# Kernel tuning notes

Measured on AMD Instinct MI355X. Metric: run time of the kernel, lower is better.

The kernel has to match this reference:

```python
import jax, jax.numpy as jnp
import numpy as np
from jax import lax

BN_EPS = 1e-5


def setup_inputs() -> dict:
    key = jax.random.key(0)
    ks = jax.random.split(key, 3)
    B, N, D = 96, 20, 2048
    return {
        "x": jax.random.normal(ks[0], (B, N, D), dtype=jnp.float32),
        "conv_w": jax.random.normal(ks[1], (D, 2 * D), dtype=jnp.float32) * 0.02,
        "conv_b": jax.random.normal(ks[2], (D,), dtype=jnp.float32) * 0.02,
        "bn_gamma": jnp.ones((D,), dtype=jnp.float32),
        "bn_beta": jnp.zeros((D,), dtype=jnp.float32),
        "bn_mean": jnp.zeros((D,), dtype=jnp.float32),
        "bn_var": jnp.ones((D,), dtype=jnp.float32),
        "n_neighbor": 10,
    }


def reference(x, conv_w, conv_b, bn_gamma, bn_beta, bn_mean, bn_var, n_neighbor):
    # x: [B, N, D] -> xt: [B, D, N] (channels-first point cloud of view features)
    xt = jnp.transpose(x, (0, 2, 1))
    B, D, N = xt.shape
    k = int(n_neighbor)

    # pairwise squared distances: [B, N, N]
    sq = jnp.sum(xt * xt, axis=1, keepdims=True)            # [B, 1, N]
    inner = jnp.einsum("bdn,bdm->bnm", xt, xt)              # [B, N, N]
    adj = sq + (-2.0) * inner + jnp.transpose(sq, (0, 2, 1))

    # k nearest neighbors (smallest distance) -> idx [B, N, k]
    _, nn_idx = lax.top_k(-adj, k)

    # gather neighbor features without the O(N^2) expand: [B, D, N, k]
    neighbors = jax.vmap(lambda xb, idx: xb[:, idx])(xt, nn_idx)

    center = xt[:, :, :, None]                              # [B, D, N, 1]
    edge = jnp.concatenate(
        [jnp.broadcast_to(center, (B, D, N, k)), neighbors - center], axis=1
    )                                                       # [B, 2D, N, k]

    # 1x1 conv (GEMM over channel dim) + BatchNorm (inference) + ReLU
    y = jnp.einsum("oc,bcnk->bonk", conv_w, edge) + conv_b[None, :, None, None]
    inv = bn_gamma / jnp.sqrt(bn_var + BN_EPS)
    y = y * inv[None, :, None, None] + (bn_beta - bn_mean * inv)[None, :, None, None]
    y = jax.nn.relu(y)

    # max over neighbors, then max over points -> [B, D, 1, 1]
    y = jnp.max(y, axis=-1, keepdims=True)
    y = jnp.max(y, axis=2, keepdims=True)
    return y
```

## Files before the change

kernel.cpp:

```cpp
#include <hip/hip_runtime.h>
#include <hip/hip_bf16.h>
#include <math.h>

#define BN_EPS 1e-5f
#define B_  96
#define N_  20
#define D_  2048
#define K_  10
#define M_  (B_*N_)
#define R_  (2*D_)

typedef __attribute__((ext_vector_type(8))) short bf16x8;
typedef __attribute__((ext_vector_type(4))) float f32x4;
typedef __attribute__((ext_vector_type(8))) unsigned short ushort8;

static __device__ __forceinline__ unsigned short f2bf(float f) {
  unsigned int u = __builtin_bit_cast(unsigned int, f);
  u = u + 0x7fffu + ((u >> 16) & 1u);
  return (unsigned short)(u >> 16);
}

#define GLOAD_LDS16(g, l) \
  __builtin_amdgcn_global_load_lds((const __attribute__((address_space(1))) void*)(g), \
                                   (__attribute__((address_space(3))) void*)(l), 16, 0, 0)

__global__ __launch_bounds__(512) void knn_cast_kernel(const float* __restrict__ x,
                                                       int* __restrict__ nn_idx,
                                                       unsigned short* __restrict__ Xb)
{
  int b = blockIdx.x, t = threadIdx.x, w = t >> 6, lane = t & 63;
  __shared__ float innr[N_*N_];
  __shared__ float adjl[N_*N_];
  const float* xb = x + (size_t)b * N_ * D_;
  for (int p = w; p < (N_*(N_+1))/2; p += 8) {
    int n = 0;
    while ((n+1)*N_ - ((n+1)*n)/2 <= p) ++n;
    int m = n + (p - (n*N_ - (n*(n-1))/2));
    const float4* xn = (const float4*)(xb + n * D_);
    const float4* xm = (const float4*)(xb + m * D_);
    float s = 0.f;
    #pragma unroll
    for (int c = lane; c < D_/4; c += 64) {
      float4 a = xn[c], v = xm[c];
      s = fmaf(a.x, v.x, fmaf(a.y, v.y, fmaf(a.z, v.z, fmaf(a.w, v.w, s))));
    }
    #pragma unroll
    for (int off = 32; off > 0; off >>= 1)
      s += __shfl_xor(s, off, 64);
    if (lane == 0) { innr[n*N_+m] = s; innr[m*N_+n] = s; }
  }
  __syncthreads();
  for (int p = t; p < N_*N_; p += 512) {
    int n = p / N_, m = p % N_;
    adjl[p] = innr[n*N_+n] + innr[m*N_+m] - 2.f * innr[p];
  }
  __syncthreads();
  if (t < N_) {
    int n = t;
    unsigned mask = 0;
    for (int it = 0; it < K_; ++it) {
      float bv = INFINITY; int bi = 0;
      for (int m = 0; m < N_; ++m) {
        if (!((mask >> m) & 1u)) {
          float v = adjl[n*N_+m];
          if (v < bv) { bv = v; bi = m; }
        }
      }
      mask |= 1u << bi;
      nn_idx[(b*N_ + n)*K_ + it] = bi;
    }
  }
  unsigned short* xo = Xb + (size_t)b * N_ * D_;
  for (int i = t; i < N_*D_/8; i += 512) {
    const float4* src = (const float4*)xb + (size_t)i * 2;
    float4 a = src[0], c = src[1];
    ushort8 o = { f2bf(a.x), f2bf(a.y), f2bf(a.z), f2bf(a.w),
                  f2bf(c.x), f2bf(c.y), f2bf(c.z), f2bf(c.w) };
    *((ushort8*)xo + i) = o;
  }
}

__global__ __launch_bounds__(256) void cast_w_kernel(const float* __restrict__ cw,
                                                     unsigned short* __restrict__ Wn)
{
  int i = blockIdx.x * 256 + threadIdx.x;
  int r = i >> 8;
  int k = (i & 255) * 8;
  const float* src = cw + (size_t)(r >> 1) * R_ + ((r & 1) << 11) + k;
  float4 a = *(const float4*)src, c = *(const float4*)(src + 4);
  ushort8 o = { f2bf(a.x), f2bf(a.y), f2bf(a.z), f2bf(a.w),
                f2bf(c.x), f2bf(c.y), f2bf(c.z), f2bf(c.w) };
  *((ushort8*)Wn + i) = o;
}

__global__ __launch_bounds__(256, 4) void fused_gemm(
    const unsigned short* __restrict__ Xb, const unsigned short* __restrict__ Wn,
    const int* __restrict__ nn_idx, const float* __restrict__ conv_b,
    const float* __restrict__ gamma, const float* __restrict__ beta,
    const float* __restrict__ mean, const float* __restrict__ var,
    float* __restrict__ out)
{
  __shared__ __align__(16) char smem[44160];
  unsigned short* As = (unsigned short*)smem;
  unsigned short* Bs = (unsigned short*)(smem + 10240);
  float* Cl  = (float*)smem;
  int*   idxl = (int*)(smem + 40960);

  int flat = blockIdx.y * 24 + blockIdx.x;
  int nf = (flat & 7) * 96 + (flat >> 3);
  int bx = nf % 24, by = nf / 24;

  int t = threadIdx.x, lane = t & 63, w = t >> 6;
  int m0 = bx * 80, b0 = bx * 4;
  int r0 = by * 128, o0 = by * 64;
  int rowsel = lane & 15, ksel = lane >> 4;

  for (int i = t; i < 4*N_*K_; i += 256) idxl[i] = nn_idx[b0*N_*K_ + i];

  f32x4 acc[5][2] = {};

  for (int k0 = 0; k0 < D_; k0 += 64) {
    #pragma unroll
    for (int i = 0; i < 3; ++i) {
      int fl = i*256 + t;
      if (fl < 640) {
        int row = fl >> 3, kc = fl & 7;
        GLOAD_LDS16(Xb + (size_t)(m0 + row) * D_ + k0 + ((kc ^ (row & 7)) << 3),
                    As + fl*8);
      }
    }
    #pragma unroll
    for (int i = 0; i < 4; ++i) {
      int fl = i*256 + t;
      int row = fl >> 3, kc = fl & 7;
      GLOAD_LDS16(Wn + (size_t)(r0 + row) * D_ + k0 + ((kc ^ (row & 7)) << 3),
                  Bs + fl*8);
    }
    __syncthreads();
    #pragma unroll
    for (int ks = 0; ks < 2; ++ks) {
      int swz = ((ks*4 + ksel) ^ (rowsel & 7)) << 3;
      bf16x8 a[5], bfr[2];
      #pragma unroll
      for (int mi = 0; mi < 5; ++mi)
        a[mi] = *(const bf16x8*)(As + (mi*16 + rowsel)*64 + swz);
      #pragma unroll
      for (int ri = 0; ri < 2; ++ri)
        bfr[ri] = *(const bf16x8*)(Bs + (w*32 + ri*16 + rowsel)*64 + swz);
      #pragma unroll
      for (int mi = 0; mi < 5; ++mi)
        #pragma unroll
        for (int ri = 0; ri < 2; ++ri)
          acc[mi][ri] = __builtin_amdgcn_mfma_f32_16x16x32_bf16(a[mi], bfr[ri], acc[mi][ri], 0, 0, 0);
    }
    __syncthreads();
  }

  #pragma unroll
  for (int mi = 0; mi < 5; ++mi)
    #pragma unroll
    for (int ri = 0; ri < 2; ++ri)
      #pragma unroll
      for (int rg = 0; rg < 4; ++rg)
        Cl[(mi*16 + ksel*4 + rg)*128 + w*32 + ri*16 + rowsel] = acc[mi][ri][rg];
  __syncthreads();

  int bb = w, oo = lane;
  int og = o0 + oo;
  float invv  = gamma[og] / sqrtf(var[og] + BN_EPS);
  float shift = fmaf(-mean[og], invv, beta[og]);
  float bias  = conv_b[og];
  float best = 0.f;
  int rbase = bb * N_;
  for (int n = 0; n < N_; ++n) {
    float Pv = Cl[(rbase + n)*128 + oo*2];
    float Qn = Cl[(rbase + n)*128 + oo*2 + 1];
    float aa = Pv - Qn + bias;
    const int* ix = idxl + bb*N_*K_ + n*K_;
    #pragma unroll
    for (int kk = 0; kk < K_; ++kk) {
      int j = ix[kk];
      float v = fmaf(aa + Cl[(rbase + j)*128 + oo*2 + 1], invv, shift);
      best = fmaxf(best, v);
    }
  }
  out[(size_t)(b0 + bb) * D_ + og] = best;
}

extern "C" void kernel_launch(void* const* d_in, const int* in_sizes, int n_in,
                              void* d_out, int out_size, void* d_ws, size_t ws_size,
                              hipStream_t stream)
{
  const float* x      = (const float*)d_in[0];
  const float* conv_w = (const float*)d_in[1];
  const float* conv_b = (const float*)d_in[2];
  const float* gamma  = (const float*)d_in[3];
  const float* beta   = (const float*)d_in[4];
  const float* mean   = (const float*)d_in[5];
  const float* var    = (const float*)d_in[6];

  int* nn_idx = (int*)d_ws;
  unsigned short* Xb = (unsigned short*)((char*)d_ws + 76800);
  unsigned short* Wn = (unsigned short*)((char*)d_ws + 76800 + (size_t)M_*D_*2);

  knn_cast_kernel<<<B_, 512, 0, stream>>>(x, nn_idx, Xb);
  cast_w_kernel<<<(R_*D_/8)/256, 256, 0, stream>>>(conv_w, Wn);
  fused_gemm<<<dim3(24, 32), 256, 0, stream>>>(
      Xb, Wn, nn_idx, conv_b, gamma, beta, mean, var, (float*)d_out);
}
```

Baseline: 92.89 us.

## Double-buffer GEMM K-tiles and merge weight cast into the kNN prep kernel

The GEMM main loop now uses a K-step of 32 with two LDS buffers. Global-to-LDS loads for the next tile are issued while MFMAs run on the current one, which halves the barrier-exposed load latency per step. The separate weight-cast kernel is folded into the kNN/X-cast kernel as extra blocks, saving one launch and letting both casts run concurrently. The cost is a smaller per-stage tile with more loop iterations and barriers, plus a 4-way swizzle that may cause more LDS bank conflicts.

```diff
diff --git a/kernel.cpp b/kernel.cpp
--- a/kernel.cpp
+++ b/kernel.cpp
@@ -24,11 +24,27 @@
   __builtin_amdgcn_global_load_lds((const __attribute__((address_space(1))) void*)(g), \
                                    (__attribute__((address_space(3))) void*)(l), 16, 0, 0)
 
-__global__ __launch_bounds__(512) void knn_cast_kernel(const float* __restrict__ x,
-                                                       int* __restrict__ nn_idx,
-                                                       unsigned short* __restrict__ Xb)
+__global__ __launch_bounds__(512) void prep_kernel(const float* __restrict__ x,
+                                                   const float* __restrict__ cw,
+                                                   int* __restrict__ nn_idx,
+                                                   unsigned short* __restrict__ Xb,
+                                                   unsigned short* __restrict__ Wn)
 {
-  int b = blockIdx.x, t = threadIdx.x, w = t >> 6, lane = t & 63;
+  int t = threadIdx.x;
+  if (blockIdx.x >= B_) {
+    int cb = blockIdx.x - B_;
+    for (int i = cb*512 + t; i < R_*D_/8; i += 416*512) {
+      int r = i >> 8;
+      int k = (i & 255) * 8;
+      const float* src = cw + (size_t)(r >> 1) * R_ + ((r & 1) << 11) + k;
+      float4 a = *(const float4*)src, c = *(const float4*)(src + 4);
+      ushort8 o = { f2bf(a.x), f2bf(a.y), f2bf(a.z), f2bf(a.w),
+                    f2bf(c.x), f2bf(c.y), f2bf(c.z), f2bf(c.w) };
+      *((ushort8*)Wn + i) = o;
+    }
+    return;
+  }
+  int b = blockIdx.x, w = t >> 6, lane = t & 63;
   __shared__ float innr[N_*N_];
   __shared__ float adjl[N_*N_];
   const float* xb = x + (size_t)b * N_ * D_;
@@ -80,19 +96,6 @@
   }
 }
 
-__global__ __launch_bounds__(256) void cast_w_kernel(const float* __restrict__ cw,
-                                                     unsigned short* __restrict__ Wn)
-{
-  int i = blockIdx.x * 256 + threadIdx.x;
-  int r = i >> 8;
-  int k = (i & 255) * 8;
-  const float* src = cw + (size_t)(r >> 1) * R_ + ((r & 1) << 11) + k;
-  float4 a = *(const float4*)src, c = *(const float4*)(src + 4);
-  ushort8 o = { f2bf(a.x), f2bf(a.y), f2bf(a.z), f2bf(a.w),
-                f2bf(c.x), f2bf(c.y), f2bf(c.z), f2bf(c.w) };
-  *((ushort8*)Wn + i) = o;
-}
-
 __global__ __launch_bounds__(256, 4) void fused_gemm(
     const unsigned short* __restrict__ Xb, const unsigned short* __restrict__ Wn,
     const int* __restrict__ nn_idx, const float* __restrict__ conv_b,
@@ -102,7 +105,6 @@
 {
   __shared__ __align__(16) char smem[44160];
   unsigned short* As = (unsigned short*)smem;
-  unsigned short* Bs = (unsigned short*)(smem + 10240);
   float* Cl  = (float*)smem;
   int*   idxl = (int*)(smem + 40960);
 
@@ -119,40 +121,54 @@
 
   f32x4 acc[5][2] = {};
 
-  for (int k0 = 0; k0 < D_; k0 += 64) {
-    #pragma unroll
-    for (int i = 0; i < 3; ++i) {
+  auto stage = [&](int bufsel, int k0) {
+    unsigned short* Asb = As + bufsel * 6656;
+    unsigned short* Bsb = Asb + 2560;
+    {
+      int row = t >> 2, kc = t & 3;
+      GLOAD_LDS16(Xb + (size_t)(m0 + row) * D_ + k0 + ((kc ^ (row & 3)) << 3),
+                  Asb + t*8);
+      if (t < 64) {
+        int fl = 256 + t, row2 = fl >> 2, kc2 = fl & 3;
+        GLOAD_LDS16(Xb + (size_t)(m0 + row2) * D_ + k0 + ((kc2 ^ (row2 & 3)) << 3),
+                    Asb + fl*8);
+      }
+    }
+    #pragma unroll
+    for (int i = 0; i < 2; ++i) {
       int fl = i*256 + t;
-      if (fl < 640) {
-        int row = fl >> 3, kc = fl & 7;
-        GLOAD_LDS16(Xb + (size_t)(m0 + row) * D_ + k0 + ((kc ^ (row & 7)) << 3),
-                    As + fl*8);
-      }
-    }
-    #pragma unroll
-    for (int i = 0; i < 4; ++i) {
-      int fl = i*256 + t;
-      int row = fl >> 3, kc = fl & 7;
-      GLOAD_LDS16(Wn + (size_t)(r0 + row) * D_ + k0 + ((kc ^ (row & 7)) << 3),
-                  Bs + fl*8);
-    }
-    __syncthreads();
-    #pragma unroll
-    for (int ks = 0; ks < 2; ++ks) {
-      int swz = ((ks*4 + ksel) ^ (rowsel & 7)) << 3;
-      bf16x8 a[5], bfr[2];
-      #pragma unroll
-      for (int mi = 0; mi < 5; ++mi)
-        a[mi] = *(const bf16x8*)(As + (mi*16 + rowsel)*64 + swz);
+      int row = fl >> 2, kc = fl & 3;
+      GLOAD_LDS16(Wn + (size_t)(r0 + row) * D_ + k0 + ((kc ^ (row & 3)) << 3),
+                  Bsb + fl*8);
+    }
+  };
+
+  auto compute = [&](int bufsel) {
+    unsigned short* Asb = As + bufsel * 6656;
+    unsigned short* Bsb = Asb + 2560;
+    int swz = (ksel ^ (rowsel & 3)) << 3;
+    bf16x8 a[5], bv[2];
+    #pragma unroll
+    for (int mi = 0; mi < 5; ++mi)
+      a[mi] = *(const bf16x8*)(Asb + (mi*16 + rowsel)*32 + swz);
+    #pragma unroll
+    for (int ri = 0; ri < 2; ++ri)
+      bv[ri] = *(const bf16x8*)(Bsb + (w*32 + ri*16 + rowsel)*32 + swz);
+    #pragma unroll
+    for (int mi = 0; mi < 5; ++mi)
       #pragma unroll
       for (int ri = 0; ri < 2; ++ri)
-        bfr[ri] = *(const bf16x8*)(Bs + (w*32 + ri*16 + rowsel)*64 + swz);
-      #pragma unroll
-      for (int mi = 0; mi < 5; ++mi)
-        #pragma unroll
-        for (int ri = 0; ri < 2; ++ri)
-          acc[mi][ri] = __builtin_amdgcn_mfma_f32_16x16x32_bf16(a[mi], bfr[ri], acc[mi][ri], 0, 0, 0);
-    }
+        acc[mi][ri] = __builtin_amdgcn_mfma_f32_16x16x32_bf16(a[mi], bv[ri], acc[mi][ri], 0, 0, 0);
+  };
+
+  stage(0, 0);
+  __syncthreads();
+  for (int kt = 0; kt < D_/32; kt += 2) {
+    stage(1, (kt+1)*32);
+    compute(0);
+    __syncthreads();
+    if (kt + 2 < D_/32) stage(0, (kt+2)*32);
+    compute(1);
     __syncthreads();
   }
 
@@ -203,8 +219,7 @@
   unsigned short* Xb = (unsigned short*)((char*)d_ws + 76800);
   unsigned short* Wn = (unsigned short*)((char*)d_ws + 76800 + (size_t)M_*D_*2);
 
-  knn_cast_kernel<<<B_, 512, 0, stream>>>(x, nn_idx, Xb);
-  cast_w_kernel<<<(R_*D_/8)/256, 256, 0, stream>>>(conv_w, Wn);
+  prep_kernel<<<B_ + 416, 512, 0, stream>>>(x, conv_w, nn_idx, Xb, Wn);
   fused_gemm<<<dim3(24, 32), 256, 0, stream>>>(
       Xb, Wn, nn_idx, conv_b, gamma, beta, mean, var, (float*)d_out);
 }
```

Result: slower. 104.3 us (+12.2%).
